# Kernel optimization log

Measured on AMD Instinct MI355X. Metric: run time of the kernel, lower is better.

The kernel has to match this reference:

```python
import jax, jax.numpy as jnp
import numpy as np
from jax import lax

PAD = 1
T, B, V, E, H, K = 256, 64, 50000, 300, 256, 20  # H = hidden_dim//2 per direction


def setup_inputs() -> dict:
    key = jax.random.key(0)
    ks = jax.random.split(key, 14)
    lengths = jnp.sort(jax.random.randint(ks[0], (B,), T // 2, T + 1))[::-1]  # sorted desc like pack_padded
    toks = jax.random.randint(ks[1], (T, B), 2, V)
    tpos = jnp.arange(T)[:, None]
    x = jnp.where(tpos < lengths[None, :], toks, PAD)
    n = jax.random.normal
    s = 1.0 / np.sqrt(H)
    emb = (n(ks[2], (V, E)) * 0.1).at[PAD].set(0.0)  # padding_idx row zeroed
    Wih0 = n(ks[3], (2, 4 * H, E)) * s       # [dir, 4H, in]
    Whh0 = n(ks[4], (2, 4 * H, H)) * s
    b0 = n(ks[5], (2, 4 * H)) * s            # b_ih + b_hh folded together
    Wih1 = n(ks[6], (2, 4 * H, 2 * H)) * s
    Whh1 = n(ks[7], (2, 4 * H, H)) * s
    b1 = n(ks[8], (2, 4 * H)) * s
    W_out = n(ks[9], (K, 2 * H)) * s
    b_out = n(ks[10], (K,)) * s
    trans = n(ks[11], (K, K)) * 0.1
    start = n(ks[12], (K,)) * 0.1
    end = n(ks[13], (K,)) * 0.1
    return dict(x=x, sent_lengths=lengths, emb=emb, Wih0=Wih0, Whh0=Whh0, b0=b0,
                Wih1=Wih1, Whh1=Whh1, b1=b1, W_out=W_out, b_out=b_out,
                trans=trans, start=start, end=end)


def _lstm_dir(xs, m, Wih, Whh, b):
    # xs [T,B,D], m [T,B,1] float mask. PyTorch gate order i,f,g,o.
    xg = jnp.einsum('tbd,gd->tbg', xs, Wih) + b  # big GEMM up-front
    h0 = jnp.zeros((xs.shape[1], H), xs.dtype)

    def step(carry, inp):
        h, c = carry
        g_t, m_t = inp
        gates = g_t + h @ Whh.T
        i, f, g, o = jnp.split(gates, 4, -1)
        c_new = jax.nn.sigmoid(f) * c + jax.nn.sigmoid(i) * jnp.tanh(g)
        h_new = jax.nn.sigmoid(o) * jnp.tanh(c_new)
        # freeze state at padded steps (pack_padded semantics); padded outputs are zero
        return (jnp.where(m_t > 0, h_new, h), jnp.where(m_t > 0, c_new, c)), h_new * m_t

    _, out = lax.scan(step, (h0, h0), (xg, m))
    return out


def _bilstm(xs, m, rev, Wih, Whh, b):
    out_f = _lstm_dir(xs, m, Wih[0], Whh[0], b[0])
    xs_r = jnp.take_along_axis(xs, rev[:, :, None], 0)  # reverse within each length
    out_b = jnp.take_along_axis(_lstm_dir(xs_r, m, Wih[1], Whh[1], b[1]), rev[:, :, None], 0)
    return jnp.concatenate([out_f, out_b], -1)


def reference(x, sent_lengths, emb, Wih0, Whh0, b0, Wih1, Whh1, b1, W_out, b_out, trans, start, end):
    mask = x != PAD                               # [T,B]
    m = mask[:, :, None].astype(emb.dtype)
    tpos = jnp.arange(T)[:, None]
    rev = jnp.where(tpos < sent_lengths[None, :], sent_lengths[None, :] - 1 - tpos, tpos)
    h = emb[x]                                    # [T,B,E]
    h = _bilstm(h, m, rev, Wih0, Whh0, b0)
    h = _bilstm(h, m, rev, Wih1, Whh1, b1)
    emis = jnp.einsum('tbh,kh->tbk', h, W_out) + b_out  # [T,B,K]

    # Viterbi decode (torchcrf semantics)
    score0 = start[None, :] + emis[0]             # [B,K]

    def vstep(sc, inp):
        e_t, m_t = inp
        cand = sc[:, :, None] + trans[None] + e_t[:, None, :]  # [B,prev,next]
        best = cand.max(1)
        ptr = cand.argmax(1).astype(jnp.int32)
        sc2 = jnp.where(m_t[:, None], best, sc)
        # identity pointer at padded steps so backtrace passes tags through
        ptr = jnp.where(m_t[:, None], ptr, jnp.arange(K, dtype=jnp.int32)[None, :])
        return sc2, ptr

    score, hist = lax.scan(vstep, score0, (emis[1:], mask[1:]))
    score = score + end[None, :]                  # score frozen at seq end -> same as adding at last valid step
    last = jnp.argmax(score, -1).astype(jnp.int32)

    def back(tag, ptr):
        prev = jnp.take_along_axis(ptr, tag[:, None], 1)[:, 0]
        return prev, prev

    _, tags_prev = lax.scan(back, last, hist, reverse=True)
    tags = jnp.concatenate([tags_prev, last[None, :]], 0)  # [T,B]
    return jnp.where(mask, tags, 0)
```

## Files before the change

### kernel.cpp

```cpp
#include <hip/hip_runtime.h>
#include <stdint.h>


#define T_ 256
#define B_ 64
#define EPAD 304
#define KTAG 20
#define TB_ (T_ * B_)
#define RES 80
#define NQ 44


__global__ void prep_embed(const int* __restrict__ x, const float* __restrict__ emb,
                           float* __restrict__ xsA) {
  int r = blockIdx.x;
  int tok = x[r];
  const float* src = emb + (size_t)tok * 300;
  for (int e = threadIdx.x; e < EPAD; e += 64)
    xsA[(size_t)r * EPAD + e] = (e < 300) ? src[e] : 0.f;
}

__global__ void prep_b0t(const float* __restrict__ Wih0, float* __restrict__ B0t) {
  int idx = blockIdx.x * 256 + threadIdx.x;
  if (idx >= 2048 * EPAD) return;
  int n = idx / EPAD, k = idx % EPAD;
  B0t[idx] = (k < 300) ? Wih0[(size_t)n * 300 + k] : 0.f;
}

__global__ void prep_bot64(const float* __restrict__ Wout, float* __restrict__ Bot,
                           const float* __restrict__ bout, float* __restrict__ biaso) {
  int idx = blockIdx.x * 256 + threadIdx.x;
  int n = idx >> 9, k = idx & 511;
  Bot[idx] = (n < KTAG) ? Wout[(size_t)n * 512 + k] : 0.f;
  if (idx < 64) biaso[idx] = (idx < KTAG) ? bout[idx] : 0.f;
}

__global__ void prep_whh2(const float* __restrict__ Whh, float* __restrict__ whhL) {
  int idx = blockIdx.x * 256 + threadIdx.x;
  int d = idx >> 18, rem = idx & 262143, k = rem >> 10, tg = rem & 1023;
  int row = (tg & 3) * 256 + (tg >> 2);
  float v = Whh[(size_t)d * 262144 + (size_t)row * 256 + k];
  if (k < RES) whhL[(size_t)(d * RES + k) * 1024 + tg] = v;
  else {
    int kk = k - RES, q = kk >> 2, e = kk & 3;
    whhL[(size_t)2 * RES * 1024 + ((size_t)(d * NQ + q) * 1024 + tg) * 4 + e] = v;
  }
}

__global__ __launch_bounds__(256) void gemm_f32(
    const float* __restrict__ A, int lda, const float* __restrict__ Bt, int ldb,
    float* __restrict__ C, int ldc, const float* __restrict__ bias,
    int ntn, int K) {
  const int tm = blockIdx.x / ntn, tn = blockIdx.x % ntn;
  const int m0 = tm * 64, n0 = tn * 64;
  __shared__ __align__(16) float As[16][64];
  __shared__ __align__(16) float Bs[16][64];
  const int tid = threadIdx.x;
  const int mm = tid >> 2, kq = (tid & 3) * 4;
  const int tx = tid & 15, ty = tid >> 4;
  float acc[4][4] = {};
  for (int k0 = 0; k0 < K; k0 += 16) {
    float4 av = *(const float4*)&A[(size_t)(m0 + mm) * lda + k0 + kq];
    float4 bv = *(const float4*)&Bt[(size_t)(n0 + mm) * ldb + k0 + kq];
    __syncthreads();
    As[kq + 0][mm] = av.x; As[kq + 1][mm] = av.y;
    As[kq + 2][mm] = av.z; As[kq + 3][mm] = av.w;
    Bs[kq + 0][mm] = bv.x; Bs[kq + 1][mm] = bv.y;
    Bs[kq + 2][mm] = bv.z; Bs[kq + 3][mm] = bv.w;
    __syncthreads();
#pragma unroll
    for (int kk = 0; kk < 16; ++kk) {
      float4 a4 = *(const float4*)&As[kk][ty * 4];
      float4 b4 = *(const float4*)&Bs[kk][tx * 4];
      acc[0][0] += a4.x * b4.x; acc[0][1] += a4.x * b4.y;
      acc[0][2] += a4.x * b4.z; acc[0][3] += a4.x * b4.w;
      acc[1][0] += a4.y * b4.x; acc[1][1] += a4.y * b4.y;
      acc[1][2] += a4.y * b4.z; acc[1][3] += a4.y * b4.w;
      acc[2][0] += a4.z * b4.x; acc[2][1] += a4.z * b4.y;
      acc[2][2] += a4.z * b4.z; acc[2][3] += a4.z * b4.w;
      acc[3][0] += a4.w * b4.x; acc[3][1] += a4.w * b4.y;
      acc[3][2] += a4.w * b4.z; acc[3][3] += a4.w * b4.w;
    }
  }
#pragma unroll
  for (int i = 0; i < 4; ++i)
#pragma unroll
    for (int j = 0; j < 4; ++j)
      C[(size_t)(m0 + ty * 4 + i) * ldc + n0 + tx * 4 + j] =
          acc[i][j] + bias[n0 + tx * 4 + j];
}

__global__ __launch_bounds__(1024) void lstm_rec(
    const float* __restrict__ xg, const float* __restrict__ whhL,
    float* __restrict__ out, const int* __restrict__ lens) {
  const int wg = blockIdx.x, dir = wg & 1, b = wg >> 1;
  const int len = lens[b];
  const int tg = threadIdx.x;
  const int j = tg >> 2, gt = tg & 3;
  const int xrow = gt * 256 + j;

  float wres[RES];
#pragma unroll
  for (int p = 0; p < RES; ++p)
    wres[p] = whhL[(size_t)(dir * RES + p) * 1024 + tg];
  const float* sp = whhL + (size_t)2 * RES * 1024 + ((size_t)dir * NQ * 1024 + tg) * 4;

  __shared__ __align__(16) float hsd[2][256];
  if (tg < 256) hsd[0][tg] = 0.f;
  float c = 0.f;
  __syncthreads();

  const int lane = tg & 63, qb = lane & ~3;

  for (int s = 0; s < len; ++s) {
    const int t = dir ? (len - 1 - s) : s;
    const int r = t * B_ + b;
    float xv = xg[(size_t)r * 2048 + dir * 1024 + xrow];
    const float4* Hr = (const float4*)hsd[s & 1];
    float a = 0.f;
#pragma unroll
    for (int p = 0; p < RES / 4; ++p) {
      float4 h4 = Hr[p];
      a += wres[4 * p] * h4.x + wres[4 * p + 1] * h4.y +
           wres[4 * p + 2] * h4.z + wres[4 * p + 3] * h4.w;
    }
#pragma unroll 4
    for (int q = 0; q < NQ; ++q) {
      float4 wv = *(const float4*)(sp + (size_t)q * 4096);
      float4 h4 = Hr[RES / 4 + q];
      a += wv.x * h4.x + wv.y * h4.y + wv.z * h4.z + wv.w * h4.w;
    }
    a += xv;
    float v1 = __shfl(a, qb | 1);
    float v2 = __shfl(a, qb | 2);
    float v3 = __shfl(a, qb | 3);
    if (gt == 0) {
      float si = 1.f / (1.f + expf(-a));
      float sf = 1.f / (1.f + expf(-v1));
      float so = 1.f / (1.f + expf(-v3));
      c = sf * c + si * tanhf(v2);
      float h = so * tanhf(c);
      hsd[(s + 1) & 1][j] = h;
      out[(size_t)r * 512 + dir * 256 + j] = h;
    }
    __syncthreads();
  }
  for (int t = len; t < T_; ++t)
    if (gt == 0) out[(size_t)(t * B_ + b) * 512 + dir * 256 + j] = 0.f;
}

__global__ __launch_bounds__(64) void viterbi(
    const float* __restrict__ emis, const float* __restrict__ trans,
    const float* __restrict__ startv, const float* __restrict__ endv,
    const int* __restrict__ lens, int* __restrict__ outp) {
  int b = blockIdx.x, lane = threadIdx.x;
  __shared__ float tr[KTAG * KTAG];
  __shared__ float fin[KTAG];
  __shared__ unsigned char hist[T_ * KTAG];
  for (int i = lane; i < KTAG * KTAG; i += 64) tr[i] = trans[i];
  int len = lens[b];
  float score = (lane < KTAG) ? startv[lane] + emis[(size_t)b * 64 + lane] : -3e38f;
  __syncthreads();
  for (int t = 1; t < len; ++t) {
    float e = (lane < KTAG) ? emis[(size_t)(t * B_ + b) * 64 + lane] : 0.f;
    float best = -3e38f; int bp = 0;
    for (int p = 0; p < KTAG; ++p) {
      float cand = (__shfl(score, p) + tr[p * KTAG + lane]) + e;
      if (cand > best) { best = cand; bp = p; }
    }
    if (lane < KTAG) { score = best; hist[t * KTAG + lane] = (unsigned char)bp; }
  }
  if (lane < KTAG) fin[lane] = score + endv[lane];
  __syncthreads();
  if (lane == 0) {
    float bb = -3e38f; int tag = 0;
    for (int p = 0; p < KTAG; ++p)
      if (fin[p] > bb) { bb = fin[p]; tag = p; }
    for (int t = len - 1; t >= 1; --t) {
      outp[t * B_ + b] = tag;
      tag = hist[t * KTAG + tag];
    }
    outp[b] = tag;
  }
  for (int t = len + lane; t < T_; t += 64) outp[t * B_ + b] = 0;
}

__global__ void sentinel_fill(int* __restrict__ outp, int val) {
  int i = blockIdx.x * 256 + threadIdx.x;
  if (i < TB_) outp[i] = val;
}
__global__ void diag_init(int* __restrict__ f) { if (threadIdx.x == 0) f[0] = 0; }
__global__ void check_nan(const float* __restrict__ p, long n, int* __restrict__ f) {
  long i0 = (long)blockIdx.x * 256 + threadIdx.x;
  int bad = 0;
  for (long i = i0; i < n; i += (long)gridDim.x * 256)
    if (!(fabsf(p[i]) <= 1e8f)) bad = 1;
  if (bad) atomicOr(&f[0], 1);
}
__global__ void verdict(const int* __restrict__ f, int* __restrict__ outp) {
  if (f[0]) outp[threadIdx.x] = -4096;
}


extern "C" void kernel_launch(void* const* d_in, const int* in_sizes, int n_in,
                              void* d_out, int out_size, void* d_ws, size_t ws_size,
                              hipStream_t stream) {
  int* outp = (int*)d_out;

  static const int exp_sizes[14] = {16384, 64, 15000000, 614400, 524288, 2048,
                                    1048576, 524288, 2048, 10240, 20, 400, 20, 20};
  int badi = (n_in == 14) ? -1 : 14;
  if (badi < 0)
    for (int i = 0; i < 14; ++i)
      if (in_sizes[i] != exp_sizes[i]) { badi = i; break; }
  if (badi >= 0) {
    hipLaunchKernelGGL(sentinel_fill, dim3((TB_ + 255) / 256), dim3(256), 0, stream,
                       outp, -(20000 + badi));
    return;
  }

  const int*   x      = (const int*)d_in[0];
  const int*   lens   = (const int*)d_in[1];
  const float* emb    = (const float*)d_in[2];
  const float* Wih0   = (const float*)d_in[3];
  const float* Whh0   = (const float*)d_in[4];
  const float* b0     = (const float*)d_in[5];
  const float* Wih1   = (const float*)d_in[6];
  const float* Whh1   = (const float*)d_in[7];
  const float* b1     = (const float*)d_in[8];
  const float* Wout   = (const float*)d_in[9];
  const float* bout   = (const float*)d_in[10];
  const float* trans  = (const float*)d_in[11];
  const float* startv = (const float*)d_in[12];
  const float* endv   = (const float*)d_in[13];

  const size_t sz_whh = (size_t)(2 * RES * 1024 + 2 * NQ * 1024 * 4) * 4;

  const size_t need =
      (size_t)TB_ * 2048 * 4
    + (size_t)TB_ * EPAD * 4
    + (size_t)TB_ * 512 * 4
    + (size_t)2048 * EPAD * 4
    + (size_t)64 * 512 * 4
    + 2 * sz_whh
    + 64 * 4
    + (size_t)TB_ * 64 * 4
    + 64;

  if (ws_size < need) {
    hipLaunchKernelGGL(sentinel_fill, dim3((TB_ + 255) / 256), dim3(256), 0, stream,
                       outp, -(int)(10000 + (ws_size >> 20)));
    return;
  }

  char* w = (char*)d_ws;
  float* xg    = (float*)w;  w += (size_t)TB_ * 2048 * 4;
  float* xsA   = (float*)w;  w += (size_t)TB_ * EPAD * 4;
  float* outh  = (float*)w;  w += (size_t)TB_ * 512 * 4;
  float* B0t   = (float*)w;  w += (size_t)2048 * EPAD * 4;
  float* Bot   = (float*)w;  w += (size_t)64 * 512 * 4;
  float* whh0L = (float*)w;  w += sz_whh;
  float* whh1L = (float*)w;  w += sz_whh;
  float* biaso = (float*)w;  w += 64 * 4;
  float* emis  = (float*)w;  w += (size_t)TB_ * 64 * 4;
  int*   diag  = (int*)w;    w += 64;

  hipLaunchKernelGGL(diag_init, dim3(1), dim3(64), 0, stream, diag);
  hipLaunchKernelGGL(prep_embed, dim3(TB_), dim3(64), 0, stream, x, emb, xsA);
  hipLaunchKernelGGL(prep_b0t, dim3((2048 * EPAD + 255) / 256), dim3(256), 0, stream, Wih0, B0t);
  hipLaunchKernelGGL(prep_bot64, dim3(128), dim3(256), 0, stream, Wout, Bot, bout, biaso);
  hipLaunchKernelGGL(prep_whh2, dim3(2048), dim3(256), 0, stream, Whh0, whh0L);
  hipLaunchKernelGGL(prep_whh2, dim3(2048), dim3(256), 0, stream, Whh1, whh1L);

  hipLaunchKernelGGL(gemm_f32, dim3(256 * 32), dim3(256), 0, stream,
                     xsA, EPAD, B0t, EPAD, xg, 2048, b0, 32, EPAD);
  hipLaunchKernelGGL(lstm_rec, dim3(128), dim3(1024), 0, stream, xg, whh0L, outh, lens);
  hipLaunchKernelGGL(gemm_f32, dim3(256 * 32), dim3(256), 0, stream,
                     outh, 512, Wih1, 512, xg, 2048, b1, 32, 512);
  hipLaunchKernelGGL(lstm_rec, dim3(128), dim3(1024), 0, stream, xg, whh1L, outh, lens);
  hipLaunchKernelGGL(gemm_f32, dim3(256), dim3(256), 0, stream,
                     outh, 512, Bot, 512, emis, 64, biaso, 1, 512);
  hipLaunchKernelGGL(check_nan, dim3(256), dim3(256), 0, stream,
                     emis, (long)TB_ * 64, diag);
  hipLaunchKernelGGL(viterbi, dim3(B_), dim3(64), 0, stream,
                     emis, trans, startv, endv, lens, outp);
  hipLaunchKernelGGL(verdict, dim3(1), dim3(64), 0, stream, diag, outp);
}
```

Measured before the change: 4.501 ms.

## Split LSTM recurrent matvec over k-quarters with all four gates per thread

The recurrent kernel's work split changes. Each thread now computes all four gate partials (i,f,g,o) for one hidden unit over a quarter of the k dimension, and the partials are reduced with xor shuffles instead of gathering gate values from neighbouring lanes. Whh is re-laid out as float4 per (k, thread). About 20 k-values live in registers, 9 are staged in LDS (144KB), and the rest stream from global memory. The h buffer is padded to avoid LDS bank conflicts. This aims to cut the per-step global weight traffic, in exchange for a large LDS footprint and extra shuffle reductions.

Result: slower. 8.957 ms (+99.0%).

```diff
diff --git a/kernel.cpp b/kernel.cpp
--- a/kernel.cpp
+++ b/kernel.cpp
@@ -7,8 +7,6 @@
 #define EPAD 304
 #define KTAG 20
 #define TB_ (T_ * B_)
-#define RES 80
-#define NQ 44
 
 
 __global__ void prep_embed(const int* __restrict__ x, const float* __restrict__ emb,
@@ -35,16 +33,12 @@
   if (idx < 64) biaso[idx] = (idx < KTAG) ? bout[idx] : 0.f;
 }
 
-__global__ void prep_whh2(const float* __restrict__ Whh, float* __restrict__ whhL) {
+__global__ void prep_whh3(const float* __restrict__ Whh, float* __restrict__ whhL) {
   int idx = blockIdx.x * 256 + threadIdx.x;
-  int d = idx >> 18, rem = idx & 262143, k = rem >> 10, tg = rem & 1023;
-  int row = (tg & 3) * 256 + (tg >> 2);
-  float v = Whh[(size_t)d * 262144 + (size_t)row * 256 + k];
-  if (k < RES) whhL[(size_t)(d * RES + k) * 1024 + tg] = v;
-  else {
-    int kk = k - RES, q = kk >> 2, e = kk & 3;
-    whhL[(size_t)2 * RES * 1024 + ((size_t)(d * NQ + q) * 1024 + tg) * 4 + e] = v;
-  }
+  int m = idx & 3, tg = (idx >> 2) & 1023, kl = (idx >> 12) & 63, d = idx >> 18;
+  int gq = tg >> 2, kq = tg & 3;
+  int row = m * 256 + gq, k = kq * 64 + kl;
+  whhL[idx] = Whh[(size_t)d * 262144 + (size_t)row * 256 + k];
 }
 
 __global__ __launch_bounds__(256) void gemm_f32(
@@ -90,63 +84,72 @@
           acc[i][j] + bias[n0 + tx * 4 + j];
 }
 
-__global__ __launch_bounds__(1024) void lstm_rec(
+__global__ __launch_bounds__(1024, 4) void lstm_rec(
     const float* __restrict__ xg, const float* __restrict__ whhL,
     float* __restrict__ out, const int* __restrict__ lens) {
   const int wg = blockIdx.x, dir = wg & 1, b = wg >> 1;
   const int len = lens[b];
   const int tg = threadIdx.x;
-  const int j = tg >> 2, gt = tg & 3;
-  const int xrow = gt * 256 + j;
-
-  float wres[RES];
-#pragma unroll
-  for (int p = 0; p < RES; ++p)
-    wres[p] = whhL[(size_t)(dir * RES + p) * 1024 + tg];
-  const float* sp = whhL + (size_t)2 * RES * 1024 + ((size_t)dir * NQ * 1024 + tg) * 4;
-
-  __shared__ __align__(16) float hsd[2][256];
-  if (tg < 256) hsd[0][tg] = 0.f;
+  const int gq = tg >> 2, kq = tg & 3;
+
+  const float4* W4 = (const float4*)whhL;
+  float4 wres[20];
+#pragma unroll
+  for (int p = 0; p < 20; ++p)
+    wres[p] = W4[(size_t)(dir * 64 + p) * 1024 + tg];
+
+  __shared__ __align__(16) float4 wlds[9 * 1024];
+  __shared__ __align__(16) float hs[2][272];
+#pragma unroll
+  for (int q = 0; q < 9; ++q)
+    wlds[q * 1024 + tg] = W4[(size_t)(dir * 64 + 20 + q) * 1024 + tg];
+  if (tg < 544) ((float*)hs)[tg] = 0.f;
   float c = 0.f;
   __syncthreads();
 
-  const int lane = tg & 63, qb = lane & ~3;
+  const float4* sp4 = W4 + (size_t)(dir * 64 + 29) * 1024 + tg;
+  const float* xbase = xg + dir * 1024 + kq * 256 + gq;
+  const int hw = (gq >> 6) * 68 + (gq & 63);
 
   for (int s = 0; s < len; ++s) {
     const int t = dir ? (len - 1 - s) : s;
     const int r = t * B_ + b;
-    float xv = xg[(size_t)r * 2048 + dir * 1024 + xrow];
-    const float4* Hr = (const float4*)hsd[s & 1];
-    float a = 0.f;
-#pragma unroll
-    for (int p = 0; p < RES / 4; ++p) {
-      float4 h4 = Hr[p];
-      a += wres[4 * p] * h4.x + wres[4 * p + 1] * h4.y +
-           wres[4 * p + 2] * h4.z + wres[4 * p + 3] * h4.w;
-    }
-#pragma unroll 4
-    for (int q = 0; q < NQ; ++q) {
-      float4 wv = *(const float4*)(sp + (size_t)q * 4096);
-      float4 h4 = Hr[RES / 4 + q];
-      a += wv.x * h4.x + wv.y * h4.y + wv.z * h4.z + wv.w * h4.w;
-    }
-    a += xv;
-    float v1 = __shfl(a, qb | 1);
-    float v2 = __shfl(a, qb | 2);
-    float v3 = __shfl(a, qb | 3);
-    if (gt == 0) {
-      float si = 1.f / (1.f + expf(-a));
-      float sf = 1.f / (1.f + expf(-v1));
-      float so = 1.f / (1.f + expf(-v3));
-      c = sf * c + si * tanhf(v2);
+    float xv = xbase[(size_t)r * 2048];
+    const float4* H4 = (const float4*)(hs[s & 1] + kq * 68);
+    float a0 = (kq == 0) ? xv : 0.f;
+    float a1 = (kq == 1) ? xv : 0.f;
+    float a2 = (kq == 2) ? xv : 0.f;
+    float a3 = (kq == 3) ? xv : 0.f;
+#pragma unroll
+    for (int grp = 0; grp < 16; ++grp) {
+      float4 h4 = H4[grp];
+#pragma unroll
+      for (int e = 0; e < 4; ++e) {
+        const int k = grp * 4 + e;
+        float4 wv = (k < 20) ? wres[k < 20 ? k : 0]
+                  : (k < 29) ? wlds[(k - 20) * 1024 + tg]
+                             : sp4[(size_t)(k - 29) * 1024];
+        float he = (e == 0) ? h4.x : (e == 1) ? h4.y : (e == 2) ? h4.z : h4.w;
+        a0 += wv.x * he; a1 += wv.y * he; a2 += wv.z * he; a3 += wv.w * he;
+      }
+    }
+    a0 += __shfl_xor(a0, 1); a1 += __shfl_xor(a1, 1);
+    a2 += __shfl_xor(a2, 1); a3 += __shfl_xor(a3, 1);
+    a0 += __shfl_xor(a0, 2); a1 += __shfl_xor(a1, 2);
+    a2 += __shfl_xor(a2, 2); a3 += __shfl_xor(a3, 2);
+    if (kq == 0) {
+      float si = 1.f / (1.f + expf(-a0));
+      float sf = 1.f / (1.f + expf(-a1));
+      float so = 1.f / (1.f + expf(-a3));
+      c = sf * c + si * tanhf(a2);
       float h = so * tanhf(c);
-      hsd[(s + 1) & 1][j] = h;
-      out[(size_t)r * 512 + dir * 256 + j] = h;
+      hs[(s + 1) & 1][hw] = h;
+      out[(size_t)r * 512 + dir * 256 + gq] = h;
     }
     __syncthreads();
   }
   for (int t = len; t < T_; ++t)
-    if (gt == 0) out[(size_t)(t * B_ + b) * 512 + dir * 256 + j] = 0.f;
+    if (kq == 0) out[(size_t)(t * B_ + b) * 512 + dir * 256 + gq] = 0.f;
 }
 
 __global__ __launch_bounds__(64) void viterbi(
@@ -234,7 +237,7 @@
   const float* startv = (const float*)d_in[12];
   const float* endv   = (const float*)d_in[13];
 
-  const size_t sz_whh = (size_t)(2 * RES * 1024 + 2 * NQ * 1024 * 4) * 4;
+  const size_t sz_whh = (size_t)524288 * 4;
 
   const size_t need =
       (size_t)TB_ * 2048 * 4
@@ -269,8 +272,8 @@
   hipLaunchKernelGGL(prep_embed, dim3(TB_), dim3(64), 0, stream, x, emb, xsA);
   hipLaunchKernelGGL(prep_b0t, dim3((2048 * EPAD + 255) / 256), dim3(256), 0, stream, Wih0, B0t);
   hipLaunchKernelGGL(prep_bot64, dim3(128), dim3(256), 0, stream, Wout, Bot, bout, biaso);
-  hipLaunchKernelGGL(prep_whh2, dim3(2048), dim3(256), 0, stream, Whh0, whh0L);
-  hipLaunchKernelGGL(prep_whh2, dim3(2048), dim3(256), 0, stream, Whh1, whh1L);
+  hipLaunchKernelGGL(prep_whh3, dim3(2048), dim3(256), 0, stream, Whh0, whh0L);
+  hipLaunchKernelGGL(prep_whh3, dim3(2048), dim3(256), 0, stream, Whh1, whh1L);
 
   hipLaunchKernelGGL(gemm_f32, dim3(256 * 32), dim3(256), 0, stream,
                      xsA, EPAD, B0t, EPAD, xg, 2048, b0, 32, EPAD);
```
